# Kernel tuning notes

Measured on AMD Instinct MI355X. Metric: run time of the kernel, lower is better.

The kernel has to match this reference:

```python
import jax, jax.numpy as jnp
import numpy as np

MIN_BIN_WIDTH = 1e-3
MIN_BIN_HEIGHT = 1e-3
MIN_DERIVATIVE = 1e-3
TAIL_BOUND = 10.0
EPS = 1e-6  # matches nflows searchsorted eps on the last bin edge
B, D, K = 32768, 512, 10


def setup_inputs() -> dict:
    key = jax.random.key(0)
    k1, k2, k3, k4 = jax.random.split(key, 4)
    return {
        # scale so some elements fall outside the +/- tail_bound linear tails
        "x": jax.random.normal(k1, (B, D), jnp.float32) * 4.0,
        "unnormalized_widths": jax.random.uniform(k2, (D, K), jnp.float32),
        "unnormalized_heights": jax.random.uniform(k3, (D, K), jnp.float32),
        "unnormalized_derivatives": jax.random.uniform(k4, (D, K - 1), jnp.float32),
    }


def _rqs_forward(x, uw, uh, ud):
    """Unconstrained rational-quadratic spline, forward direction.
    x: [B, D]; uw/uh: [D, K]; ud: [D, K-1]. Params shared across batch.
    Returns (y [B, D], logdet [B]).
    """
    left = -TAIL_BOUND
    right = TAIL_BOUND

    # normalized bin widths / cumulative x-knots  [D, K] / [D, K+1]
    w = jax.nn.softmax(uw, axis=-1)
    w = MIN_BIN_WIDTH + (1.0 - MIN_BIN_WIDTH * K) * w
    cw = jnp.concatenate([jnp.zeros((D, 1), w.dtype), jnp.cumsum(w, -1)], -1)
    cw = (right - left) * cw + left
    cw = cw.at[:, 0].set(left).at[:, -1].set(right)
    w = cw[:, 1:] - cw[:, :-1]

    # normalized bin heights / cumulative y-knots
    h = jax.nn.softmax(uh, axis=-1)
    h = MIN_BIN_HEIGHT + (1.0 - MIN_BIN_HEIGHT * K) * h
    ch = jnp.concatenate([jnp.zeros((D, 1), h.dtype), jnp.cumsum(h, -1)], -1)
    ch = (right - left) * ch + left
    ch = ch.at[:, 0].set(left).at[:, -1].set(right)
    h = ch[:, 1:] - ch[:, :-1]

    # boundary derivatives padded with softplus^{-1}(1 - min_derivative)
    const = np.log(np.exp(1.0 - MIN_DERIVATIVE) - 1.0).astype(np.float32)
    pad = jnp.full((D, 1), const, ud.dtype)
    d = MIN_DERIVATIVE + jax.nn.softplus(jnp.concatenate([pad, ud, pad], -1))  # [D, K+1]

    inside = (x >= left) & (x <= right)
    xc = jnp.clip(x, left, right)  # tails handled by identity below

    # per-element bin search (last edge bumped by EPS, as in nflows)
    cw_s = cw.at[:, -1].add(EPS)
    idx = jnp.sum(xc[..., None] >= cw_s[None], axis=-1) - 1  # [B, D]
    idx = jnp.clip(idx, 0, K - 1)

    feat = jnp.arange(D)[None, :]  # broadcast with idx [B, D]
    in_cw = cw[feat, idx]
    in_w = w[feat, idx]
    in_ch = ch[feat, idx]
    in_h = h[feat, idx]
    delta = h / w
    in_delta = delta[feat, idx]
    in_d = d[feat, idx]
    in_dp1 = d[feat, idx + 1]

    theta = (xc - in_cw) / in_w
    t1m = theta * (1.0 - theta)
    numerator = in_h * (in_delta * theta**2 + in_d * t1m)
    denominator = in_delta + (in_d + in_dp1 - 2.0 * in_delta) * t1m
    y = in_ch + numerator / denominator

    deriv_num = in_delta**2 * (in_dp1 * theta**2 + 2.0 * in_delta * t1m + in_d * (1.0 - theta) ** 2)
    lad = jnp.log(deriv_num) - 2.0 * jnp.log(denominator)

    y = jnp.where(inside, y, x)          # linear tails: identity
    lad = jnp.where(inside, lad, 0.0)    # logabsdet 0 in tails
    return y, jnp.sum(lad, axis=1)


def reference(x, unnormalized_widths, unnormalized_heights, unnormalized_derivatives):
    return _rqs_forward(x, unnormalized_widths, unnormalized_heights, unnormalized_derivatives)
```

## Files before the change

### kernel.cpp

```cpp
#include <hip/hip_runtime.h>

#define NB 32768
#define ND 512
#define NK 10

#define LEFTB (-10.0f)
#define RIGHTB (10.0f)
#define ROWS 8
#define NBLK 512

#define OFF_CWCH (9 * ND)
#define OFF_DD   (OFF_CWCH + 22 * ND)

__global__ void rqs_precompute(const float* __restrict__ uw,
                               const float* __restrict__ uh,
                               const float* __restrict__ ud,
                               float* __restrict__ ws) {
    int f = blockIdx.x * blockDim.x + threadIdx.x;
    if (f >= ND) return;

    float* E = ws;
    float2* GCWCH = (float2*)(ws + OFF_CWCH);
    float* GDD = ws + OFF_DD;

    float cw[NK + 1], ch[NK + 1], dd[NK + 1];

    {
        float u[NK];
        float m = -1e30f;
#pragma unroll
        for (int k = 0; k < NK; ++k) { u[k] = uw[f * NK + k]; m = fmaxf(m, u[k]); }
        float s = 0.0f;
#pragma unroll
        for (int k = 0; k < NK; ++k) { u[k] = expf(u[k] - m); s += u[k]; }
        float inv = 1.0f / s;
        float c = 0.0f;
        cw[0] = LEFTB;
#pragma unroll
        for (int k = 0; k < NK; ++k) {
            c += 1e-3f + (1.0f - 1e-3f * NK) * (u[k] * inv);
            cw[k + 1] = (RIGHTB - LEFTB) * c + LEFTB;
        }
        cw[NK] = RIGHTB;
    }
    {
        float u[NK];
        float m = -1e30f;
#pragma unroll
        for (int k = 0; k < NK; ++k) { u[k] = uh[f * NK + k]; m = fmaxf(m, u[k]); }
        float s = 0.0f;
#pragma unroll
        for (int k = 0; k < NK; ++k) { u[k] = expf(u[k] - m); s += u[k]; }
        float inv = 1.0f / s;
        float c = 0.0f;
        ch[0] = LEFTB;
#pragma unroll
        for (int k = 0; k < NK; ++k) {
            c += 1e-3f + (1.0f - 1e-3f * NK) * (u[k] * inv);
            ch[k + 1] = (RIGHTB - LEFTB) * c + LEFTB;
        }
        ch[NK] = RIGHTB;
    }
    dd[0] = 1.0f;
    dd[NK] = 1.0f;
#pragma unroll
    for (int k = 1; k < NK; ++k) {
        float v = ud[f * (NK - 1) + (k - 1)];
        dd[k] = 1e-3f + fmaxf(v, 0.0f) + log1pf(expf(-fabsf(v)));
    }

#pragma unroll
    for (int j = 0; j < 9; ++j) E[j * ND + f] = cw[j + 1];
#pragma unroll
    for (int k = 0; k <= NK; ++k) {
        GCWCH[k * ND + f] = make_float2(cw[k], ch[k]);
        GDD[k * ND + f] = dd[k];
    }
}

__device__ __forceinline__ float dpp_row_reduce16(float v) {
    v += __int_as_float(__builtin_amdgcn_update_dpp(
        0, __float_as_int(v), 0x111, 0xF, 0xF, true));
    v += __int_as_float(__builtin_amdgcn_update_dpp(
        0, __float_as_int(v), 0x112, 0xF, 0xF, true));
    v += __int_as_float(__builtin_amdgcn_update_dpp(
        0, __float_as_int(v), 0x114, 0xF, 0xF, true));
    v += __int_as_float(__builtin_amdgcn_update_dpp(
        0, __float_as_int(v), 0x118, 0xF, 0xF, true));
    return v;
}

__global__ __launch_bounds__(512) void rqs_main(const float* __restrict__ X,
                                                const float* __restrict__ ws,
                                                float* __restrict__ Y,
                                                float* __restrict__ logdet) {
    const int t = threadIdx.x;

    __shared__ float2 sCWCH[NK + 1][ND];
    __shared__ float sDD[NK + 1][ND];
    __shared__ float sPart[ROWS][32];

    const float* E = ws;
    const float2* GCWCH = (const float2*)(ws + OFF_CWCH);
    const float* GDD = ws + OFF_DD;

#pragma unroll
    for (int k = 0; k <= NK; ++k) {
        sCWCH[k][t] = GCWCH[k * ND + t];
        sDD[k][t] = GDD[k * ND + t];
    }
    float e[9];
#pragma unroll
    for (int j = 0; j < 9; ++j) e[j] = E[j * ND + t];
    __syncthreads();

    for (int r0 = blockIdx.x * ROWS; r0 < NB; r0 += NBLK * ROWS) {
        float xs[ROWS], ys[ROWS], ls[ROWS];
#pragma unroll
        for (int i = 0; i < ROWS; ++i)
            xs[i] = __builtin_nontemporal_load(&X[(r0 + i) * ND + t]);

#pragma unroll
        for (int i = 0; i < ROWS; ++i) {
            float x = xs[i];

            int idx = 0;
#pragma unroll
            for (int j = 0; j < 9; ++j) idx += (x >= e[j]) ? 1 : 0;

            float2 c0 = sCWCH[idx][t];
            float2 c1 = sCWCH[idx + 1][t];
            float dk = sDD[idx][t];
            float dk1 = sDD[idx + 1][t];

            float w = c1.x - c0.x;
            float rw = __builtin_amdgcn_rcpf(w);
            float h = c1.y - c0.y;
            float delta = h * rw;

            float theta = (x - c0.x) * rw;
            float omt = 1.0f - theta;
            float t1m = theta * omt;
            float th2 = theta * theta;

            float num = h * fmaf(delta, th2, dk * t1m);
            float den = fmaf(fmaf(-2.0f, delta, dk + dk1), t1m, delta);
            float rden = __builtin_amdgcn_rcpf(den);
            float y = fmaf(num, rden, c0.y);

            float dnum = delta * delta *
                         (fmaf(dk1, th2, 2.0f * delta * t1m) + dk * omt * omt);
            float lad2 = __log2f(dnum * rden * rden);

            bool inside = fabsf(x) <= RIGHTB;
            ys[i] = inside ? y : x;
            ls[i] = inside ? lad2 : 0.0f;
        }

#pragma unroll
        for (int i = 0; i < ROWS; ++i)
            __builtin_nontemporal_store(ys[i], &Y[(r0 + i) * ND + t]);

#pragma unroll
        for (int i = 0; i < ROWS; ++i) ls[i] = dpp_row_reduce16(ls[i]);
        if ((t & 15) == 15) {
            int g = t >> 4;
#pragma unroll
            for (int i = 0; i < ROWS; ++i) sPart[i][g] = ls[i];
        }
        __syncthreads();

        if (t < 256) {
            float v = ((const float*)sPart)[t];
            v += __shfl_xor(v, 1, 32);
            v += __shfl_xor(v, 2, 32);
            v += __shfl_xor(v, 4, 32);
            v += __shfl_xor(v, 8, 32);
            v += __shfl_xor(v, 16, 32);
            if ((t & 31) == 0)
                logdet[r0 + (t >> 5)] = v * 0.6931471805599453f;
        }
        __syncthreads();
    }
}

extern "C" void kernel_launch(void* const* d_in, const int* in_sizes, int n_in,
                              void* d_out, int out_size, void* d_ws, size_t ws_size,
                              hipStream_t stream) {
    const float* x  = (const float*)d_in[0];
    const float* uw = (const float*)d_in[1];
    const float* uh = (const float*)d_in[2];
    const float* ud = (const float*)d_in[3];

    float* out = (float*)d_out;
    float* Y = out;
    float* logdet = out + (size_t)NB * ND;

    float* ws = (float*)d_ws;

    hipLaunchKernelGGL(rqs_precompute, dim3(4), dim3(128), 0, stream,
                       uw, uh, ud, ws);
    hipLaunchKernelGGL(rqs_main, dim3(NBLK), dim3(ND), 0, stream,
                       x, ws, Y, logdet);
}
```

Measured before the change: 43.06 us.

## Prefetch next sweep's rows and defer logdet reduction to one final pass

```diff
diff --git a/kernel.cpp b/kernel.cpp
--- a/kernel.cpp
+++ b/kernel.cpp
@@ -8,6 +8,7 @@
 #define RIGHTB (10.0f)
 #define ROWS 8
 #define NBLK 512
+#define SWEEPS (NB / (NBLK * ROWS))
 
 #define OFF_CWCH (9 * ND)
 #define OFF_DD   (OFF_CWCH + 22 * ND)
@@ -98,7 +99,7 @@
 
     __shared__ float2 sCWCH[NK + 1][ND];
     __shared__ float sDD[NK + 1][ND];
-    __shared__ float sPart[ROWS][32];
+    __shared__ float sPart[SWEEPS * ROWS][32] __attribute__((aligned(16)));
 
     const float* E = ws;
     const float2* GCWCH = (const float2*)(ws + OFF_CWCH);
@@ -114,12 +115,26 @@
     for (int j = 0; j < 9; ++j) e[j] = E[j * ND + t];
     __syncthreads();
 
-    for (int r0 = blockIdx.x * ROWS; r0 < NB; r0 += NBLK * ROWS) {
-        float xs[ROWS], ys[ROWS], ls[ROWS];
+    float xs[ROWS];
+    {
+        const int rb = blockIdx.x * ROWS;
 #pragma unroll
         for (int i = 0; i < ROWS; ++i)
-            xs[i] = __builtin_nontemporal_load(&X[(r0 + i) * ND + t]);
-
+            xs[i] = __builtin_nontemporal_load(&X[(rb + i) * ND + t]);
+    }
+
+    for (int it = 0; it < SWEEPS; ++it) {
+        const int rb = blockIdx.x * ROWS + it * (NBLK * ROWS);
+
+        float xn[ROWS];
+        if (it + 1 < SWEEPS) {
+            const int rn = rb + NBLK * ROWS;
+#pragma unroll
+            for (int i = 0; i < ROWS; ++i)
+                xn[i] = __builtin_nontemporal_load(&X[(rn + i) * ND + t]);
+        }
+
+        float ys[ROWS], ls[ROWS];
 #pragma unroll
         for (int i = 0; i < ROWS; ++i) {
             float x = xs[i];
@@ -159,28 +174,35 @@
 
 #pragma unroll
         for (int i = 0; i < ROWS; ++i)
-            __builtin_nontemporal_store(ys[i], &Y[(r0 + i) * ND + t]);
+            __builtin_nontemporal_store(ys[i], &Y[(rb + i) * ND + t]);
 
 #pragma unroll
         for (int i = 0; i < ROWS; ++i) ls[i] = dpp_row_reduce16(ls[i]);
         if ((t & 15) == 15) {
             int g = t >> 4;
 #pragma unroll
-            for (int i = 0; i < ROWS; ++i) sPart[i][g] = ls[i];
-        }
-        __syncthreads();
-
-        if (t < 256) {
-            float v = ((const float*)sPart)[t];
-            v += __shfl_xor(v, 1, 32);
-            v += __shfl_xor(v, 2, 32);
-            v += __shfl_xor(v, 4, 32);
-            v += __shfl_xor(v, 8, 32);
-            v += __shfl_xor(v, 16, 32);
-            if ((t & 31) == 0)
-                logdet[r0 + (t >> 5)] = v * 0.6931471805599453f;
-        }
-        __syncthreads();
+            for (int i = 0; i < ROWS; ++i) sPart[it * ROWS + i][g] = ls[i];
+        }
+
+#pragma unroll
+        for (int i = 0; i < ROWS; ++i) xs[i] = xn[i];
+    }
+
+    __syncthreads();
+    {
+        const int rl = t >> 3;
+        const int c = t & 7;
+        const int it = rl >> 3;
+        const int i = rl & 7;
+        float4 v4 = *(const float4*)&sPart[rl][c * 4];
+        float v = (v4.x + v4.y) + (v4.z + v4.w);
+        v += __shfl_xor(v, 1, 8);
+        v += __shfl_xor(v, 2, 8);
+        v += __shfl_xor(v, 4, 8);
+        if (c == 0) {
+            const int row = blockIdx.x * ROWS + it * (NBLK * ROWS) + i;
+            logdet[row] = v * 0.6931471805599453f;
+        }
     }
 }
 
```

After: 42.19 us. 2.0% less time.
